# Optimization experiments

Hardware: AMD Instinct MI355X
Metric: run time of the kernel (lower is better)

## Reference

```python
import jax, jax.numpy as jnp
import numpy as np

E = 2_000_000   # edges
N = 200_000     # atoms
B = 100         # bond types (10 species, ordered pairs)
R = 13          # reduced_matrix_element (SK integrals per bond)
G = 512         # num_xgrid
T = 10          # atom types
OE = 4          # n_onsite_Es
R_MIN, R_MAX = 1.0, 6.0  # SK table distance range (Bohr-ish)


def setup_inputs() -> dict:
    key = jax.random.key(0)
    k1, k2, k3, k4, k5, k6 = jax.random.split(key, 6)
    rij = jax.random.uniform(k1, (E,), jnp.float32, 1.5, 5.5)
    edge_type = jax.random.randint(k2, (E,), 0, B, jnp.int32)
    atom_type = jax.random.randint(k3, (N,), 0, T, jnp.int32)
    xx = jnp.linspace(R_MIN, R_MAX, G, dtype=jnp.float32)  # sorted distance grid
    hopping_param = jax.random.normal(k4, (B, R, G), jnp.float32)
    overlap_param = jax.random.normal(k5, (B, R, G), jnp.float32)
    onsite_param = jax.random.normal(k6, (T, OE, 1), jnp.float32)
    return {"rij": rij, "edge_type": edge_type, "atom_type": atom_type,
            "xx": xx, "hopping_param": hopping_param,
            "overlap_param": overlap_param, "onsite_param": onsite_param}


def _interp_by_type(rij, edge_type, xx, table):
    """Fused gather + linear interpolation, keyed by edge_type.

    Replaces the original per-bond-type masked loop: for each edge, pick the
    [R, G] SK table for its bond type and linearly interpolate along the
    distance grid at rij. Returns [E, R].
    """
    g = xx.shape[0]
    # interval index for each edge (clamped -> linear extrapolation at edges)
    idx = jnp.clip(jnp.searchsorted(xx, rij, side="right") - 1, 0, g - 2)  # [E]
    x0 = xx[idx]
    x1 = xx[idx + 1]
    t = ((rij - x0) / (x1 - x0))[:, None]  # [E, 1]
    # advanced indexing on axes 0 and 2, full slice on axis 1 -> [E, R]
    y0 = table[edge_type, :, idx]
    y1 = table[edge_type, :, idx + 1]
    return y0 * (1.0 - t) + y1 * t


def reference(rij, edge_type, atom_type, xx, hopping_param, overlap_param, onsite_param):
    edge_features = _interp_by_type(rij, edge_type, xx, hopping_param)   # [E, R]
    edge_overlap = _interp_by_type(rij, edge_type, xx, overlap_param)    # [E, R]
    # dftb onsite: direct per-atom-type parameter lookup (num_paras == 1)
    node_features = onsite_param[atom_type, :, 0]                         # [N, OE]
    return edge_features, edge_overlap, node_features
```

## Files before the change

### kernel.cpp

```cpp
#include <hip/hip_runtime.h>

#define E_CNT 2000000
#define N_CNT 200000
#define B_CNT 100
#define R_CNT 13
#define G_CNT 512
#define T_CNT 10
#define OE_CNT 4

#define P_ROWH 32
#define P_HALFS ((size_t)B_CNT * G_CNT * P_ROWH)
#define P_BYTES (P_HALFS * 2)

#define EDGES_PER_BLOCK 64
#define EDGE_BLOCKS (E_CNT / EDGES_PER_BLOCK)
#define NODE_BLOCKS ((N_CNT + 255) / 256)
#define OUT_OVL_OFF ((size_t)E_CNT * R_CNT)
#define OUT_NODE_OFF ((size_t)2 * E_CNT * R_CNT)

#define SH_STRIDE 20

typedef float v4f __attribute__((ext_vector_type(4)));
typedef _Float16 v8h __attribute__((ext_vector_type(8)));

__global__ __launch_bounds__(256) void repack_h16_kernel(
    const float* __restrict__ hopping,
    const float* __restrict__ overlap,
    _Float16* __restrict__ P)
{
    int tid = blockIdx.x * 256 + threadIdx.x;
    int b = tid >> 9;
    int g = tid & (G_CNT - 1);
    float h[13], o[13];
    #pragma unroll
    for (int r = 0; r < R_CNT; ++r) {
        size_t src = (((size_t)b * R_CNT + r) << 9) + g;
        h[r] = hopping[src];
        o[r] = overlap[src];
    }
    v8h w0, w1, w2, w3;
    #pragma unroll
    for (int k = 0; k < 8; ++k) {
        w0[k] = (_Float16)h[k];
        w1[k] = (8 + k < R_CNT) ? (_Float16)h[8 + k] : (_Float16)0.0f;
        w2[k] = (_Float16)o[k];
        w3[k] = (8 + k < R_CNT) ? (_Float16)o[8 + k] : (_Float16)0.0f;
    }
    _Float16* dst = P + (size_t)tid * P_ROWH;
    *(v8h*)(dst)      = w0;
    *(v8h*)(dst + 8)  = w1;
    *(v8h*)(dst + 16) = w2;
    *(v8h*)(dst + 24) = w3;
}

__global__ __launch_bounds__(256) void sk16_kernel(
    const float* __restrict__ rij,
    const int*   __restrict__ edge_type,
    const _Float16* __restrict__ P,
    const int*   __restrict__ atom_type,
    const float* __restrict__ onsite,
    float* __restrict__ out)
{
    if (blockIdx.x < EDGE_BLOCKS) {
        __shared__ float shh[EDGES_PER_BLOCK * SH_STRIDE];
        __shared__ float sho[EDGES_PER_BLOCK * SH_STRIDE];

        int tid = threadIdx.x;
        int eL = tid >> 2;
        int j  = tid & 3;
        int e  = blockIdx.x * EDGES_PER_BLOCK + eL;

        float r = __builtin_nontemporal_load(rij + e);
        int   b = __builtin_nontemporal_load(edge_type + e);

        const float inv_dx = 511.0f / 5.0f;
        float s = (r - 1.0f) * inv_dx;
        int idx = (int)s;
        idx = max(0, min(G_CNT - 2, idx));
        float t = s - (float)idx;
        float omt = 1.0f - t;

        const _Float16* rowp = P + ((size_t)((b << 9) + idx)) * P_ROWH + j * 8;
        v8h y0 = *(const v8h*)(rowp);
        v8h y1 = *(const v8h*)(rowp + P_ROWH);

        float vv[8];
        #pragma unroll
        for (int k = 0; k < 8; ++k)
            vv[k] = (float)y0[k] * omt + (float)y1[k] * t;

        float* shp = (j < 2 ? shh : sho) + eL * SH_STRIDE + (j & 1) * 8;
        v4f lo = { vv[0], vv[1], vv[2], vv[3] };
        v4f hi = { vv[4], vv[5], vv[6], vv[7] };
        *(v4f*)(shp)     = lo;
        *(v4f*)(shp + 4) = hi;
        __syncthreads();

        if (tid < 208) {
            unsigned f0 = (unsigned)tid * 4u;
            float ph[4], po[4];
            #pragma unroll
            for (int k = 0; k < 4; ++k) {
                unsigned f = f0 + k;
                unsigned ee = f / 13u;
                unsigned rr = f - ee * 13u;
                ph[k] = shh[ee * SH_STRIDE + rr];
                po[k] = sho[ee * SH_STRIDE + rr];
            }
            v4f qh = { ph[0], ph[1], ph[2], ph[3] };
            v4f qo = { po[0], po[1], po[2], po[3] };
            size_t ob = (size_t)blockIdx.x * (EDGES_PER_BLOCK * R_CNT) + f0;
            __builtin_nontemporal_store(qh, (v4f*)(out + ob));
            __builtin_nontemporal_store(qo, (v4f*)(out + OUT_OVL_OFF + ob));
        }
    } else {
        int n = (int)(blockIdx.x - EDGE_BLOCKS) * 256 + threadIdx.x;
        if (n < N_CNT) {
            int t = atom_type[n];
            v4f v = { onsite[t * OE_CNT + 0],
                      onsite[t * OE_CNT + 1],
                      onsite[t * OE_CNT + 2],
                      onsite[t * OE_CNT + 3] };
            __builtin_nontemporal_store(v, (v4f*)(out + OUT_NODE_OFF + (size_t)n * OE_CNT));
        }
    }
}

__global__ __launch_bounds__(256) void dftbsk_fallback(
    const float* __restrict__ rij,
    const int*   __restrict__ edge_type,
    const int*   __restrict__ atom_type,
    const float* __restrict__ xx,
    const float* __restrict__ hopping,
    const float* __restrict__ overlap,
    const float* __restrict__ onsite,
    float*       __restrict__ out)
{
    __shared__ float sxx[G_CNT];
    for (int i = threadIdx.x; i < G_CNT; i += blockDim.x) sxx[i] = xx[i];
    __syncthreads();

    long long gid = (long long)blockIdx.x * blockDim.x + threadIdx.x;
    if (gid < E_CNT) {
        int e = (int)gid;
        float r = rij[e];
        int b = edge_type[e];
        const float inv_dx = (float)(G_CNT - 1) / 5.0f;
        int idx = (int)floorf((r - 1.0f) * inv_dx);
        idx = max(0, min(G_CNT - 2, idx));
        while (idx > 0 && r < sxx[idx]) --idx;
        while (idx < G_CNT - 2 && r >= sxx[idx + 1]) ++idx;
        float x0 = sxx[idx], x1 = sxx[idx + 1];
        float t = (r - x0) / (x1 - x0);
        float omt = 1.0f - t;
        const float* hb = hopping + (size_t)b * (R_CNT * G_CNT) + idx;
        const float* ob = overlap + (size_t)b * (R_CNT * G_CNT) + idx;
        float* outh = out + (size_t)e * R_CNT;
        float* outo = out + OUT_OVL_OFF + (size_t)e * R_CNT;
        #pragma unroll
        for (int rr = 0; rr < R_CNT; ++rr)
            outh[rr] = hb[rr * G_CNT] * omt + hb[rr * G_CNT + 1] * t;
        #pragma unroll
        for (int rr = 0; rr < R_CNT; ++rr)
            outo[rr] = ob[rr * G_CNT] * omt + ob[rr * G_CNT + 1] * t;
    } else if (gid < (long long)E_CNT + N_CNT) {
        int n = (int)(gid - E_CNT);
        int t = atom_type[n];
        float4 v;
        v.x = onsite[t * OE_CNT + 0];
        v.y = onsite[t * OE_CNT + 1];
        v.z = onsite[t * OE_CNT + 2];
        v.w = onsite[t * OE_CNT + 3];
        *(float4*)(out + OUT_NODE_OFF + (size_t)n * OE_CNT) = v;
    }
}

extern "C" void kernel_launch(void* const* d_in, const int* in_sizes, int n_in,
                              void* d_out, int out_size, void* d_ws, size_t ws_size,
                              hipStream_t stream) {
    const float* rij        = (const float*)d_in[0];
    const int*   edge_type  = (const int*)d_in[1];
    const int*   atom_type  = (const int*)d_in[2];
    const float* xx         = (const float*)d_in[3];
    const float* hopping    = (const float*)d_in[4];
    const float* overlap    = (const float*)d_in[5];
    const float* onsite     = (const float*)d_in[6];
    float* out = (float*)d_out;

    if (ws_size >= P_BYTES) {
        _Float16* P = (_Float16*)d_ws;
        repack_h16_kernel<<<(B_CNT * G_CNT) / 256, 256, 0, stream>>>(
            hopping, overlap, P);
        sk16_kernel<<<EDGE_BLOCKS + NODE_BLOCKS, 256, 0, stream>>>(
            rij, edge_type, P, atom_type, onsite, out);
    } else {
        const long long total = (long long)E_CNT + N_CNT;
        const int grid = (int)((total + 255) / 256);
        dftbsk_fallback<<<grid, 256, 0, stream>>>(rij, edge_type, atom_type, xx,
                                                  hopping, overlap, onsite, out);
    }
}
```

Baseline: 256.7 us.

## Assign one edge per thread with eight 16-byte gathers for memory-level parallelism

Each thread now processes a whole edge and issues all eight fp16 row loads (both grid points for hopping and overlap) itself, instead of four threads per edge each loading two vectors. Blocks cover 256 edges, and the shared staging stride changes to 17 to avoid bank conflicts under the new layout. The store loop becomes a strided loop over the block's outputs. The aim is more outstanding loads per thread and fewer blocks. In exchange it raises register pressure and makes the per-thread row reads uncoalesced, with scalar shared-memory writes.

```diff
diff --git a/kernel.cpp b/kernel.cpp
--- a/kernel.cpp
+++ b/kernel.cpp
@@ -12,13 +12,13 @@
 #define P_HALFS ((size_t)B_CNT * G_CNT * P_ROWH)
 #define P_BYTES (P_HALFS * 2)
 
-#define EDGES_PER_BLOCK 64
-#define EDGE_BLOCKS (E_CNT / EDGES_PER_BLOCK)
+#define EPB 256
+#define EDGE_BLOCKS ((E_CNT + EPB - 1) / EPB)
 #define NODE_BLOCKS ((N_CNT + 255) / 256)
 #define OUT_OVL_OFF ((size_t)E_CNT * R_CNT)
 #define OUT_NODE_OFF ((size_t)2 * E_CNT * R_CNT)
 
-#define SH_STRIDE 20
+#define SH_STRIDE 17
 
 typedef float v4f __attribute__((ext_vector_type(4)));
 typedef _Float16 v8h __attribute__((ext_vector_type(8)));
@@ -53,7 +53,7 @@
     *(v8h*)(dst + 24) = w3;
 }
 
-__global__ __launch_bounds__(256) void sk16_kernel(
+__global__ __launch_bounds__(256, 4) void sk16_mlp_kernel(
     const float* __restrict__ rij,
     const int*   __restrict__ edge_type,
     const _Float16* __restrict__ P,
@@ -62,56 +62,64 @@
     float* __restrict__ out)
 {
     if (blockIdx.x < EDGE_BLOCKS) {
-        __shared__ float shh[EDGES_PER_BLOCK * SH_STRIDE];
-        __shared__ float sho[EDGES_PER_BLOCK * SH_STRIDE];
-
-        int tid = threadIdx.x;
-        int eL = tid >> 2;
-        int j  = tid & 3;
-        int e  = blockIdx.x * EDGES_PER_BLOCK + eL;
-
-        float r = __builtin_nontemporal_load(rij + e);
-        int   b = __builtin_nontemporal_load(edge_type + e);
-
-        const float inv_dx = 511.0f / 5.0f;
-        float s = (r - 1.0f) * inv_dx;
-        int idx = (int)s;
-        idx = max(0, min(G_CNT - 2, idx));
-        float t = s - (float)idx;
-        float omt = 1.0f - t;
-
-        const _Float16* rowp = P + ((size_t)((b << 9) + idx)) * P_ROWH + j * 8;
-        v8h y0 = *(const v8h*)(rowp);
-        v8h y1 = *(const v8h*)(rowp + P_ROWH);
-
-        float vv[8];
-        #pragma unroll
-        for (int k = 0; k < 8; ++k)
-            vv[k] = (float)y0[k] * omt + (float)y1[k] * t;
-
-        float* shp = (j < 2 ? shh : sho) + eL * SH_STRIDE + (j & 1) * 8;
-        v4f lo = { vv[0], vv[1], vv[2], vv[3] };
-        v4f hi = { vv[4], vv[5], vv[6], vv[7] };
-        *(v4f*)(shp)     = lo;
-        *(v4f*)(shp + 4) = hi;
+        __shared__ float shh[EPB * SH_STRIDE];
+        __shared__ float sho[EPB * SH_STRIDE];
+
+        int tid   = threadIdx.x;
+        int ebase = blockIdx.x * EPB;
+        int ne    = min(EPB, E_CNT - ebase);
+
+        if (tid < ne) {
+            int e = ebase + tid;
+            float r = __builtin_nontemporal_load(rij + e);
+            int   b = __builtin_nontemporal_load(edge_type + e);
+
+            const float inv_dx = 511.0f / 5.0f;
+            float s = (r - 1.0f) * inv_dx;
+            int idx = (int)s;
+            idx = max(0, min(G_CNT - 2, idx));
+            float t = s - (float)idx;
+            float omt = 1.0f - t;
+
+            const _Float16* rowp = P + ((size_t)((b << 9) + idx)) * P_ROWH;
+            v8h a0 = *(const v8h*)(rowp);
+            v8h a1 = *(const v8h*)(rowp + 8);
+            v8h a2 = *(const v8h*)(rowp + 16);
+            v8h a3 = *(const v8h*)(rowp + 24);
+            v8h b0 = *(const v8h*)(rowp + 32);
+            v8h b1 = *(const v8h*)(rowp + 40);
+            v8h b2 = *(const v8h*)(rowp + 48);
+            v8h b3 = *(const v8h*)(rowp + 56);
+
+            float* hrow = shh + tid * SH_STRIDE;
+            float* orow = sho + tid * SH_STRIDE;
+            #pragma unroll
+            for (int k = 0; k < 8; ++k) hrow[k] = (float)a0[k] * omt + (float)b0[k] * t;
+            #pragma unroll
+            for (int k = 0; k < 5; ++k) hrow[8 + k] = (float)a1[k] * omt + (float)b1[k] * t;
+            #pragma unroll
+            for (int k = 0; k < 8; ++k) orow[k] = (float)a2[k] * omt + (float)b2[k] * t;
+            #pragma unroll
+            for (int k = 0; k < 5; ++k) orow[8 + k] = (float)a3[k] * omt + (float)b3[k] * t;
+        }
         __syncthreads();
 
-        if (tid < 208) {
-            unsigned f0 = (unsigned)tid * 4u;
+        int totf = ne * R_CNT;
+        size_t obase = (size_t)ebase * R_CNT;
+        for (int f0 = tid * 4; f0 < totf; f0 += 256 * 4) {
             float ph[4], po[4];
             #pragma unroll
             for (int k = 0; k < 4; ++k) {
-                unsigned f = f0 + k;
-                unsigned ee = f / 13u;
-                unsigned rr = f - ee * 13u;
+                int f = f0 + k;
+                int ee = f / 13;
+                int rr = f - ee * 13;
                 ph[k] = shh[ee * SH_STRIDE + rr];
                 po[k] = sho[ee * SH_STRIDE + rr];
             }
             v4f qh = { ph[0], ph[1], ph[2], ph[3] };
             v4f qo = { po[0], po[1], po[2], po[3] };
-            size_t ob = (size_t)blockIdx.x * (EDGES_PER_BLOCK * R_CNT) + f0;
-            __builtin_nontemporal_store(qh, (v4f*)(out + ob));
-            __builtin_nontemporal_store(qo, (v4f*)(out + OUT_OVL_OFF + ob));
+            __builtin_nontemporal_store(qh, (v4f*)(out + obase + f0));
+            __builtin_nontemporal_store(qo, (v4f*)(out + OUT_OVL_OFF + obase + f0));
         }
     } else {
         int n = (int)(blockIdx.x - EDGE_BLOCKS) * 256 + threadIdx.x;
@@ -191,7 +199,7 @@
         _Float16* P = (_Float16*)d_ws;
         repack_h16_kernel<<<(B_CNT * G_CNT) / 256, 256, 0, stream>>>(
             hopping, overlap, P);
-        sk16_kernel<<<EDGE_BLOCKS + NODE_BLOCKS, 256, 0, stream>>>(
+        sk16_mlp_kernel<<<EDGE_BLOCKS + NODE_BLOCKS, 256, 0, stream>>>(
             rij, edge_type, P, atom_type, onsite, out);
     } else {
         const long long total = (long long)E_CNT + N_CNT;
```

Result: no change. 259.9 us (+1.2%).
